# Optimization experiments

Hardware: AMD Instinct MI355X
Metric: run time of the kernel (lower is better)

## Reference

```python
import jax, jax.numpy as jnp
import numpy as np
from jax.scipy.linalg import solve_triangular

# module hyperparameters (match init_kwargs)
NUM_EMB = 256      # num_embeddings (dictionary atoms)
EMB_DIM = 64       # embedding_dim (latent channels)
K = 4              # sparsity_level (OMP steps / stack depth)
N_BINS = 33
COEF_MAX = 2.0
COMMIT = 0.25
EPS = 1e-10
B, H, W = 32, 32, 32

CENTERS = jnp.linspace(-COEF_MAX, COEF_MAX, N_BINS)


def setup_inputs() -> dict:
    key = jax.random.key(0)
    k1, k2 = jax.random.split(key)
    z_e = jax.random.normal(k1, (B, EMB_DIM, H, W), dtype=jnp.float32)
    dictionary = jax.random.normal(k2, (EMB_DIM, NUM_EMB), dtype=jnp.float32) * 0.02
    return {"z_e": z_e, "dictionary": dictionary}


def _normalize_dict(dictionary):
    # F.normalize(dim=0): column-wise L2 normalization with eps floor
    nrm = jnp.sqrt(jnp.sum(dictionary * dictionary, axis=0, keepdims=True))
    return dictionary / jnp.maximum(nrm, EPS)


def _quantize_coeff(coeff):
    c = jnp.clip(coeff, -COEF_MAX, COEF_MAX)
    bin_f = (c + COEF_MAX) / (2.0 * COEF_MAX) * (N_BINS - 1)
    bin_idx = jnp.clip(jnp.round(bin_f).astype(jnp.int32), 0, N_BINS - 1)
    return bin_idx, CENTERS[bin_idx]


def batch_omp(X, D):
    """Batched OMP, exactly K steps (tol=-1 so no early stop).
    X: [M, N] signals (columns), D: [M, A] normalized dictionary.
    Returns support I [N, K] (selection order) and coeffs [N, K]."""
    G = D.T @ D                      # [A, A] Gram
    h_bar = (D.T @ X).T              # [N, A] correlations
    h = h_bar
    Nsig = h_bar.shape[0]
    rows = jnp.arange(Nsig)
    I_logic = jnp.zeros(h_bar.shape, dtype=bool)
    I = None
    L = None
    x_stack = None
    for k in range(K):                # static unroll over sparsity level
        index = jnp.argmax(jnp.abs(h * (~I_logic)), axis=1)   # [N]
        I_logic = I_logic.at[rows, index].set(True)
        if k == 0:
            I = index[:, None]                                 # [N,1]
            L = jnp.ones((Nsig, 1, 1), h.dtype)                # Cholesky factor
        else:
            # grow Cholesky factor: solve L w = G[I, new]
            G_stack = G[I, index[:, None]][..., None]          # [N,k,1]
            w = solve_triangular(L, G_stack, lower=True)       # [N,k,1]
            w_corner = jnp.sqrt(jnp.clip(1.0 - jnp.sum(w * w, axis=1, keepdims=True), 1e-12))
            top = jnp.concatenate([L, jnp.zeros((Nsig, k, 1), h.dtype)], axis=2)
            bot = jnp.concatenate([jnp.swapaxes(w, 1, 2), w_corner], axis=2)
            L = jnp.concatenate([top, bot], axis=1)            # [N,k+1,k+1]
            I = jnp.concatenate([I, index[:, None]], axis=1)
        # cholesky_solve: L L^T x = h_bar[:, I]
        h_stack = jnp.take_along_axis(h_bar, I, axis=1)[..., None]  # [N,k+1,1]
        y = solve_triangular(L, h_stack, lower=True)
        x_stack = solve_triangular(jnp.swapaxes(L, 1, 2), y, lower=False)  # [N,k+1,1]
        # beta = x_sel @ G[I, :]  -> update residual correlations
        G_rows = G[I]                                          # [N,k+1,A]
        beta = jnp.einsum('nk,nka->na', x_stack[..., 0], G_rows)
        h = h_bar - beta
    return I, x_stack[..., 0]


def reference(z_e, dictionary):
    Bz, C, Hh, Ww = z_e.shape
    signals = jnp.transpose(z_e, (0, 2, 3, 1)).reshape(-1, C).T   # [C, Nsig]
    Dn = _normalize_dict(dictionary)                               # [C, A]
    # OMP runs under no_grad in the original
    support, coeffs = batch_omp(jax.lax.stop_gradient(signals), jax.lax.stop_gradient(Dn))
    support = jax.lax.stop_gradient(support)
    coeffs = jax.lax.stop_gradient(coeffs)
    bin_idx, coeff_q = _quantize_coeff(coeffs)
    tokens = (support * N_BINS + bin_idx.astype(support.dtype)).reshape(Bz, Hh, Ww, K)
    atoms = Dn.T[support]                                          # [Nsig,K,C]
    recon_flat = jnp.sum(atoms * coeff_q[..., None], axis=1)       # [Nsig,C]
    z_q = jnp.transpose(recon_flat.reshape(Bz, Hh, Ww, C), (0, 3, 1, 2))
    dl_latent = jnp.mean((z_q - jax.lax.stop_gradient(z_e)) ** 2)
    e_latent = jnp.mean((jax.lax.stop_gradient(z_q) - z_e) ** 2)
    loss = dl_latent + COMMIT * e_latent
    z_q_ste = z_e + jax.lax.stop_gradient(z_q - z_e)
    return z_q_ste, loss, tokens
```

## Files before the change

kernel.cpp:

```cpp
#include <hip/hip_runtime.h>
#include <math.h>

#define NUM_EMB 256
#define EMB_DIM 64
#define KSEL 4
#define NBINS 33
#define NSIG 32768
#define SPB 16
#define NBLK (NSIG / SPB)


__global__ void norm_kernel(const float* __restrict__ dict, float* __restrict__ Dn) {
    int a = threadIdx.x;
    double s = 0.0;
    #pragma unroll 8
    for (int c = 0; c < EMB_DIM; ++c) {
        double v = (double)dict[c * NUM_EMB + a];
        s += v * v;
    }
    double inv = 1.0 / fmax(sqrt(s), 1e-10);
    #pragma unroll 8
    for (int c = 0; c < EMB_DIM; ++c)
        Dn[c * NUM_EMB + a] = (float)((double)dict[c * NUM_EMB + a] * inv);
}

__global__ void gram_kernel(const float* __restrict__ Dn, float* __restrict__ G) {
    __shared__ float ca[EMB_DIM];
    int a = blockIdx.x;
    int t = threadIdx.x;
    if (t < EMB_DIM) ca[t] = Dn[t * NUM_EMB + a];
    __syncthreads();
    double s = 0.0;
    #pragma unroll 8
    for (int c = 0; c < EMB_DIM; ++c)
        s += (double)ca[c] * (double)Dn[c * NUM_EMB + t];
    G[a * NUM_EMB + t] = (float)s;
}

__global__ __launch_bounds__(256, 4)
void omp_kernel(const float* __restrict__ z_e, const float* __restrict__ Dn,
                const float* __restrict__ G, float* __restrict__ out,
                double* __restrict__ partial) {
    __shared__ double sbuf[4][1024];
    const int t = threadIdx.x;
    const int w = t >> 6, l = t & 63;
    const int g = l >> 4, li = l & 15;
    const int n0 = blockIdx.x * SPB + w * 4;
    double* sb = sbuf[w];

    #pragma unroll
    for (int s = 0; s < 4; ++s) {
        int n = n0 + s, b = n >> 10, hw = n & 1023;
        sb[s * EMB_DIM + l] = (double)z_e[((b * EMB_DIM + l) << 10) + hw];
    }
    asm volatile("s_waitcnt lgkmcnt(0)" ::: "memory");

    double acc[4][4];
    #pragma unroll
    for (int s = 0; s < 4; ++s)
        #pragma unroll
        for (int j = 0; j < 4; ++j) acc[s][j] = 0.0;

    #pragma unroll 4
    for (int c = 0; c < EMB_DIM; ++c) {
        const float* dp = Dn + c * NUM_EMB + l;
        double d0 = (double)dp[0];
        double d1 = (double)dp[64];
        double d2 = (double)dp[128];
        double d3 = (double)dp[192];
        double z0 = sb[c], z1 = sb[EMB_DIM + c], z2 = sb[2 * EMB_DIM + c], z3 = sb[3 * EMB_DIM + c];
        acc[0][0] += d0 * z0; acc[0][1] += d1 * z0; acc[0][2] += d2 * z0; acc[0][3] += d3 * z0;
        acc[1][0] += d0 * z1; acc[1][1] += d1 * z1; acc[1][2] += d2 * z1; acc[1][3] += d3 * z1;
        acc[2][0] += d0 * z2; acc[2][1] += d1 * z2; acc[2][2] += d2 * z2; acc[2][3] += d3 * z2;
        acc[3][0] += d0 * z3; acc[3][1] += d1 * z3; acc[3][2] += d2 * z3; acc[3][3] += d3 * z3;
    }
    asm volatile("s_waitcnt lgkmcnt(0)" ::: "memory");
    #pragma unroll
    for (int s = 0; s < 4; ++s)
        #pragma unroll
        for (int j = 0; j < 4; ++j)
            sb[s * NUM_EMB + l + 64 * j] = acc[s][j];
    asm volatile("s_waitcnt lgkmcnt(0)" ::: "memory");

    const double* hb = sb + g * NUM_EMB;
    int I[KSEL];
    double Lm[KSEL][KSEL], rL[KSEL], hI[KSEL], x[KSEL];
    unsigned selbits = 0;

    #pragma unroll
    for (int k = 0; k < KSEL; ++k) {
        double bv = -1.0; int bi = 0;
        #pragma unroll
        for (int j = 0; j < 16; ++j) {
            int a = li + 16 * j;
            double h = hb[a];
            #pragma unroll
            for (int m = 0; m < k; ++m)
                h -= x[m] * (double)G[(I[m] << 8) + a];
            double v = ((selbits >> j) & 1u) ? 0.0 : fabs(h);
            if (v > bv) { bv = v; bi = a; }
        }
        #pragma unroll
        for (int off = 1; off < 16; off <<= 1) {
            double ov = __shfl_xor(bv, off);
            int    oi = __shfl_xor(bi, off);
            if (ov > bv || (ov == bv && oi < bi)) { bv = ov; bi = oi; }
        }
        if ((bi & 15) == li) selbits |= 1u << (bi >> 4);

        if (k == 0) {
            Lm[0][0] = 1.0; rL[0] = 1.0;
        } else {
            double wv[KSEL], s2 = 0.0;
            #pragma unroll
            for (int i = 0; i < k; ++i) {
                double v = (double)G[(I[i] << 8) + bi];
                #pragma unroll
                for (int j2 = 0; j2 < i; ++j2) v -= Lm[i][j2] * wv[j2];
                v *= rL[i];
                wv[i] = v; s2 += v * v;
            }
            #pragma unroll
            for (int j2 = 0; j2 < k; ++j2) Lm[k][j2] = wv[j2];
            double dg = sqrt(fmax(1.0 - s2, 1e-12));
            Lm[k][k] = dg; rL[k] = 1.0 / dg;
        }
        I[k]  = bi;
        hI[k] = hb[bi];

        double y[KSEL];
        #pragma unroll
        for (int i = 0; i <= k; ++i) {
            double v = hI[i];
            #pragma unroll
            for (int j2 = 0; j2 < i; ++j2) v -= Lm[i][j2] * y[j2];
            y[i] = v * rL[i];
        }
        #pragma unroll
        for (int i = k; i >= 0; --i) {
            double v = y[i];
            #pragma unroll
            for (int j2 = i + 1; j2 <= k; ++j2) v -= Lm[j2][i] * x[j2];
            x[i] = v * rL[i];
        }
    }

    float cq[KSEL]; int tok[KSEL];
    #pragma unroll
    for (int i = 0; i < KSEL; ++i) {
        float xf = (float)x[i];
        float cc = fminf(fmaxf(xf, -2.0f), 2.0f);
        int bin = (int)rintf((cc + 2.0f) * 8.0f);
        bin = bin < 0 ? 0 : (bin > 32 ? 32 : bin);
        cq[i]  = -2.0f + 0.125f * (float)bin;
        tok[i] = I[i] * NBINS + bin;
    }
    if (li < KSEL) {
        float tv = li == 0 ? (float)tok[0]
                 : li == 1 ? (float)tok[1]
                 : li == 2 ? (float)tok[2] : (float)tok[3];
        out[NSIG * EMB_DIM + 1 + (n0 + g) * KSEL + li] = tv;
    }

    double sq = 0.0;
    #pragma unroll
    for (int s = 0; s < 4; ++s) {
        double z = 0.0;
        #pragma unroll
        for (int i = 0; i < KSEL; ++i) {
            int   Iv  = __shfl(I[i],  s * 16);
            float cqv = __shfl(cq[i], s * 16);
            z += (double)cqv * (double)Dn[(l << 8) + Iv];
        }
        float zf = (float)z;
        int n = n0 + s, b = n >> 10, hw = n & 1023;
        int idx = ((b * EMB_DIM + l) << 10) + hw;
        out[idx] = zf;
        double d = (double)zf - (double)z_e[idx];
        sq += d * d;
    }
    #pragma unroll
    for (int off = 1; off < 64; off <<= 1)
        sq += __shfl_xor(sq, off);
    if (l == 0) partial[blockIdx.x * 4 + w] = sq;
}

__global__ void loss_kernel(const double* __restrict__ partial, float* __restrict__ out) {
    __shared__ double sh[256];
    int t = threadIdx.x;
    double s = 0.0;
    for (int i = t; i < NBLK * 4; i += 256) s += partial[i];
    sh[t] = s;
    __syncthreads();
    for (int off = 128; off > 0; off >>= 1) {
        if (t < off) sh[t] += sh[t + off];
        __syncthreads();
    }
    if (t == 0)
        out[NSIG * EMB_DIM] = (float)(1.25 * sh[0] / (double)(NSIG * EMB_DIM));
}

extern "C" void kernel_launch(void* const* d_in, const int* in_sizes, int n_in,
                              void* d_out, int out_size, void* d_ws, size_t ws_size,
                              hipStream_t stream) {
    const float* z_e  = (const float*)d_in[0];
    const float* dict = (const float*)d_in[1];
    float* out = (float*)d_out;

    float*  Dn      = (float*)d_ws;
    float*  G       = (float*)((char*)d_ws + 65536);
    double* partial = (double*)((char*)d_ws + 327680);

    norm_kernel<<<1, 256, 0, stream>>>(dict, Dn);
    gram_kernel<<<NUM_EMB, 256, 0, stream>>>(Dn, G);
    omp_kernel<<<NBLK, 256, 0, stream>>>(z_e, Dn, G, out, partial);
    loss_kernel<<<1, 256, 0, stream>>>(partial, out);
}
```

Measured before the change: 90.22 us.

## Keep correlations in registers, vectorize loads, add transposed dictionary for reconstruction

```diff
diff --git a/kernel.cpp b/kernel.cpp
--- a/kernel.cpp
+++ b/kernel.cpp
@@ -10,7 +10,8 @@
 #define NBLK (NSIG / SPB)
 
 
-__global__ void norm_kernel(const float* __restrict__ dict, float* __restrict__ Dn) {
+__global__ void norm_kernel(const float* __restrict__ dict, float* __restrict__ Dn,
+                            float* __restrict__ DnT) {
     int a = threadIdx.x;
     double s = 0.0;
     #pragma unroll 8
@@ -20,8 +21,11 @@
     }
     double inv = 1.0 / fmax(sqrt(s), 1e-10);
     #pragma unroll 8
-    for (int c = 0; c < EMB_DIM; ++c)
-        Dn[c * NUM_EMB + a] = (float)((double)dict[c * NUM_EMB + a] * inv);
+    for (int c = 0; c < EMB_DIM; ++c) {
+        float v = (float)((double)dict[c * NUM_EMB + a] * inv);
+        Dn[c * NUM_EMB + a] = v;
+        DnT[a * EMB_DIM + c] = v;
+    }
 }
 
 __global__ void gram_kernel(const float* __restrict__ Dn, float* __restrict__ G) {
@@ -39,74 +43,91 @@
 
 __global__ __launch_bounds__(256, 4)
 void omp_kernel(const float* __restrict__ z_e, const float* __restrict__ Dn,
-                const float* __restrict__ G, float* __restrict__ out,
-                double* __restrict__ partial) {
-    __shared__ double sbuf[4][1024];
+                const float* __restrict__ G, const float* __restrict__ DnT,
+                float* __restrict__ out, double* __restrict__ partial) {
+    __shared__ double zs[4][4][EMB_DIM];
     const int t = threadIdx.x;
     const int w = t >> 6, l = t & 63;
     const int g = l >> 4, li = l & 15;
     const int n0 = blockIdx.x * SPB + w * 4;
-    double* sb = sbuf[w];
-
-    #pragma unroll
-    for (int s = 0; s < 4; ++s) {
-        int n = n0 + s, b = n >> 10, hw = n & 1023;
-        sb[s * EMB_DIM + l] = (double)z_e[((b * EMB_DIM + l) << 10) + hw];
-    }
+    const int b = n0 >> 10, hw0 = n0 & 1023;
+
+    const float4 zv = *(const float4*)(z_e + (((b * EMB_DIM + l) << 10) + hw0));
+    zs[w][0][l] = (double)zv.x;
+    zs[w][1][l] = (double)zv.y;
+    zs[w][2][l] = (double)zv.z;
+    zs[w][3][l] = (double)zv.w;
     asm volatile("s_waitcnt lgkmcnt(0)" ::: "memory");
 
     double acc[4][4];
     #pragma unroll
     for (int s = 0; s < 4; ++s)
         #pragma unroll
-        for (int j = 0; j < 4; ++j) acc[s][j] = 0.0;
+        for (int r = 0; r < 4; ++r) acc[s][r] = 0.0;
 
     #pragma unroll 4
-    for (int c = 0; c < EMB_DIM; ++c) {
-        const float* dp = Dn + c * NUM_EMB + l;
-        double d0 = (double)dp[0];
-        double d1 = (double)dp[64];
-        double d2 = (double)dp[128];
-        double d3 = (double)dp[192];
-        double z0 = sb[c], z1 = sb[EMB_DIM + c], z2 = sb[2 * EMB_DIM + c], z3 = sb[3 * EMB_DIM + c];
-        acc[0][0] += d0 * z0; acc[0][1] += d1 * z0; acc[0][2] += d2 * z0; acc[0][3] += d3 * z0;
-        acc[1][0] += d0 * z1; acc[1][1] += d1 * z1; acc[1][2] += d2 * z1; acc[1][3] += d3 * z1;
-        acc[2][0] += d0 * z2; acc[2][1] += d1 * z2; acc[2][2] += d2 * z2; acc[2][3] += d3 * z2;
-        acc[3][0] += d0 * z3; acc[3][1] += d1 * z3; acc[3][2] += d2 * z3; acc[3][3] += d3 * z3;
-    }
-    asm volatile("s_waitcnt lgkmcnt(0)" ::: "memory");
-    #pragma unroll
-    for (int s = 0; s < 4; ++s)
-        #pragma unroll
-        for (int j = 0; j < 4; ++j)
-            sb[s * NUM_EMB + l + 64 * j] = acc[s][j];
-    asm volatile("s_waitcnt lgkmcnt(0)" ::: "memory");
-
-    const double* hb = sb + g * NUM_EMB;
+    for (int c = 0; c < EMB_DIM; c += 2) {
+        const float4 dA = *(const float4*)(Dn + c * NUM_EMB + 4 * l);
+        const float4 dB = *(const float4*)(Dn + (c + 1) * NUM_EMB + 4 * l);
+        double a0 = (double)dA.x, a1 = (double)dA.y, a2 = (double)dA.z, a3 = (double)dA.w;
+        double b0 = (double)dB.x, b1 = (double)dB.y, b2 = (double)dB.z, b3 = (double)dB.w;
+        #pragma unroll
+        for (int s = 0; s < 4; ++s) {
+            double2 zp = *(const double2*)&zs[w][s][c];
+            acc[s][0] += a0 * zp.x; acc[s][1] += a1 * zp.x;
+            acc[s][2] += a2 * zp.x; acc[s][3] += a3 * zp.x;
+            acc[s][0] += b0 * zp.y; acc[s][1] += b1 * zp.y;
+            acc[s][2] += b2 * zp.y; acc[s][3] += b3 * zp.y;
+        }
+    }
+
+    double hbar[16];
+    #pragma unroll
+    for (int j = 0; j < 16; ++j) {
+        int src = 4 * li + (j >> 2);
+        double t0 = __shfl(acc[0][j & 3], src);
+        double t1 = __shfl(acc[1][j & 3], src);
+        double t2 = __shfl(acc[2][j & 3], src);
+        double t3 = __shfl(acc[3][j & 3], src);
+        hbar[j] = (g < 2) ? (g == 0 ? t0 : t1) : (g == 2 ? t2 : t3);
+    }
+
     int I[KSEL];
     double Lm[KSEL][KSEL], rL[KSEL], hI[KSEL], x[KSEL];
     unsigned selbits = 0;
 
     #pragma unroll
     for (int k = 0; k < KSEL; ++k) {
-        double bv = -1.0; int bi = 0;
-        #pragma unroll
-        for (int j = 0; j < 16; ++j) {
-            int a = li + 16 * j;
-            double h = hb[a];
-            #pragma unroll
-            for (int m = 0; m < k; ++m)
-                h -= x[m] * (double)G[(I[m] << 8) + a];
-            double v = ((selbits >> j) & 1u) ? 0.0 : fabs(h);
-            if (v > bv) { bv = v; bi = a; }
+        double bv = -1.0, bh = 0.0; int bi = 0;
+        #pragma unroll
+        for (int jb = 0; jb < 4; ++jb) {
+            double h0, h1, h2, h3;
+            h0 = hbar[4 * jb + 0]; h1 = hbar[4 * jb + 1];
+            h2 = hbar[4 * jb + 2]; h3 = hbar[4 * jb + 3];
+            #pragma unroll
+            for (int m = 0; m < k; ++m) {
+                const float4 gv = *(const float4*)(G + (I[m] << 8) + 16 * li + 4 * jb);
+                h0 -= x[m] * (double)gv.x;
+                h1 -= x[m] * (double)gv.y;
+                h2 -= x[m] * (double)gv.z;
+                h3 -= x[m] * (double)gv.w;
+            }
+            #pragma unroll
+            for (int r = 0; r < 4; ++r) {
+                int j = 4 * jb + r;
+                double h = r == 0 ? h0 : r == 1 ? h1 : r == 2 ? h2 : h3;
+                double v = ((selbits >> j) & 1u) ? 0.0 : fabs(h);
+                if (v > bv) { bv = v; bi = 16 * li + j; bh = hbar[j]; }
+            }
         }
         #pragma unroll
         for (int off = 1; off < 16; off <<= 1) {
             double ov = __shfl_xor(bv, off);
             int    oi = __shfl_xor(bi, off);
-            if (ov > bv || (ov == bv && oi < bi)) { bv = ov; bi = oi; }
-        }
-        if ((bi & 15) == li) selbits |= 1u << (bi >> 4);
+            double oh = __shfl_xor(bh, off);
+            if (ov > bv || (ov == bv && oi < bi)) { bv = ov; bi = oi; bh = oh; }
+        }
+        if ((bi >> 4) == li) selbits |= 1u << (bi & 15);
 
         if (k == 0) {
             Lm[0][0] = 1.0; rL[0] = 1.0;
@@ -126,7 +147,7 @@
             Lm[k][k] = dg; rL[k] = 1.0 / dg;
         }
         I[k]  = bi;
-        hI[k] = hb[bi];
+        hI[k] = bh;
 
         double y[KSEL];
         #pragma unroll
@@ -162,23 +183,26 @@
         out[NSIG * EMB_DIM + 1 + (n0 + g) * KSEL + li] = tv;
     }
 
-    double sq = 0.0;
-    #pragma unroll
-    for (int s = 0; s < 4; ++s) {
-        double z = 0.0;
-        #pragma unroll
-        for (int i = 0; i < KSEL; ++i) {
-            int   Iv  = __shfl(I[i],  s * 16);
-            float cqv = __shfl(cq[i], s * 16);
-            z += (double)cqv * (double)Dn[(l << 8) + Iv];
-        }
-        float zf = (float)z;
-        int n = n0 + s, b = n >> 10, hw = n & 1023;
-        int idx = ((b * EMB_DIM + l) << 10) + hw;
-        out[idx] = zf;
-        double d = (double)zf - (double)z_e[idx];
-        sq += d * d;
-    }
+    double zq0 = 0.0, zq1 = 0.0, zq2 = 0.0, zq3 = 0.0;
+    #pragma unroll
+    for (int i = 0; i < KSEL; ++i) {
+        int   I0 = __shfl(I[i],  0), I1 = __shfl(I[i], 16);
+        int   I2 = __shfl(I[i], 32), I3 = __shfl(I[i], 48);
+        float c0 = __shfl(cq[i], 0), c1 = __shfl(cq[i], 16);
+        float c2 = __shfl(cq[i], 32), c3 = __shfl(cq[i], 48);
+        zq0 += (double)c0 * (double)DnT[(I0 << 6) + l];
+        zq1 += (double)c1 * (double)DnT[(I1 << 6) + l];
+        zq2 += (double)c2 * (double)DnT[(I2 << 6) + l];
+        zq3 += (double)c3 * (double)DnT[(I3 << 6) + l];
+    }
+    float4 zqv = make_float4((float)zq0, (float)zq1, (float)zq2, (float)zq3);
+    *(float4*)(out + (((b * EMB_DIM + l) << 10) + hw0)) = zqv;
+
+    double d0 = (double)zqv.x - zs[w][0][l];
+    double d1 = (double)zqv.y - zs[w][1][l];
+    double d2 = (double)zqv.z - zs[w][2][l];
+    double d3 = (double)zqv.w - zs[w][3][l];
+    double sq = d0 * d0 + d1 * d1 + d2 * d2 + d3 * d3;
     #pragma unroll
     for (int off = 1; off < 64; off <<= 1)
         sq += __shfl_xor(sq, off);
@@ -209,10 +233,11 @@
 
     float*  Dn      = (float*)d_ws;
     float*  G       = (float*)((char*)d_ws + 65536);
-    double* partial = (double*)((char*)d_ws + 327680);
-
-    norm_kernel<<<1, 256, 0, stream>>>(dict, Dn);
+    float*  DnT     = (float*)((char*)d_ws + 327680);
+    double* partial = (double*)((char*)d_ws + 393216);
+
+    norm_kernel<<<1, 256, 0, stream>>>(dict, Dn, DnT);
     gram_kernel<<<NUM_EMB, 256, 0, stream>>>(Dn, G);
-    omp_kernel<<<NBLK, 256, 0, stream>>>(z_e, Dn, G, out, partial);
+    omp_kernel<<<NBLK, 256, 0, stream>>>(z_e, Dn, G, DnT, out, partial);
     loss_kernel<<<1, 256, 0, stream>>>(partial, out);
 }
```

Measured after the change: 80.01 us. 1.13x faster.
